# Kernel tuning notes

Measured on AMD Instinct MI355X. Metric: run time of the kernel, lower is better.

## Reference

```python
import jax, jax.numpy as jnp
import numpy as np

B, N, F_IN, HID, OUT = 4096, 116, 116, 256, 2


def setup_inputs() -> dict:
    key = jax.random.key(0)
    ks = jax.random.split(key, 10)
    x = jax.random.normal(ks[0], (B, N, F_IN), dtype=jnp.float32)
    support = jax.random.uniform(ks[1], (B, N, N), dtype=jnp.float32) / N  # row-normalized-ish adjacency
    s = 0.05
    W1 = jax.random.normal(ks[2], (F_IN, HID), dtype=jnp.float32) * s
    b1 = jnp.zeros((HID,), dtype=jnp.float32)
    W2 = jax.random.normal(ks[3], (HID, OUT * 2), dtype=jnp.float32) * s
    b2 = jnp.zeros((OUT * 2,), dtype=jnp.float32)
    Wr1 = jax.random.normal(ks[4], (N * OUT * 2, 64), dtype=jnp.float32) * s
    br1 = jnp.zeros((64,), dtype=jnp.float32)
    Wr2 = jax.random.normal(ks[5], (64, OUT), dtype=jnp.float32) * s
    br2 = jnp.zeros((OUT,), dtype=jnp.float32)
    return {"x": x, "support": support, "W1": W1, "b1": b1, "W2": W2,
            "b2": b2, "Wr1": Wr1, "br1": br1, "Wr2": Wr2, "br2": br2}


def graph_conv(x, support, W, b):
    # GraphConv: activation(support @ (x @ W) + b)
    xw = jnp.einsum('bnf,fh->bnh', x, W)
    h = jnp.einsum('bnm,bmh->bnh', support, xw) + b
    return jax.nn.relu(h)


def reference(x, support, W1, b1, W2, b2, Wr1, br1, Wr2, br2):
    h = graph_conv(x, support, W1, b1)          # [B, N, HID]
    h = graph_conv(h, support, W2, b2)          # [B, N, 2*OUT]
    flat = h.reshape(h.shape[0], -1)            # [B, N*2*OUT]
    r = jax.nn.relu(flat @ Wr1 + br1)           # [B, 64]
    logits = r @ Wr2 + br2                      # [B, OUT]
    return jax.nn.log_softmax(logits, axis=-1)
```

## Files before the change

kernel.cpp:

```cpp
#include <hip/hip_runtime.h>
#include <math.h>


#define BDIM 512

constexpr int Bsz = 4096;
constexpr int Nn  = 116;
constexpr int Fin = 116;
constexpr int HID = 256;
constexpr int SK  = 136;
constexpr int NF4 = 3364;
constexpr int W1T_ELEMS = 256 * SK;
constexpr int W2T_OFF   = W1T_ELEMS;

typedef __bf16 bf16;
typedef __bf16 bf16x4 __attribute__((ext_vector_type(4)));
typedef __bf16 bf16x8 __attribute__((ext_vector_type(8)));
typedef float  floatx4 __attribute__((ext_vector_type(4)));


__global__ __launch_bounds__(1024) void prep_weights(
    const float* __restrict__ W1, const float* __restrict__ W2,
    bf16* __restrict__ WT)
{
  int j = blockIdx.x * 1024 + threadIdx.x;
  if (j < W1T_ELEMS) {
    int h = j / SK, kk = j - h * SK;
    WT[j] = (bf16)((kk < Fin) ? W1[kk * HID + h] : 0.f);
  } else if (j < W1T_ELEMS + 4 * 264) {
    int t = j - W1T_ELEMS;
    int n = t / 264, k = t - n * 264;
    WT[j] = (bf16)((k < HID) ? W2[k * 4 + n] : 0.f);
  }
}

template <bool PADS>
__device__ __attribute__((always_inline)) inline void stage_mat(
    const float* __restrict__ g, bf16* dst, int tid)
{
  for (int i = tid; i < NF4; i += BDIM) {
    int m  = i / 29;
    int kq = (i - m * 29) * 4;
    float4 u = ((const float4*)g)[i];
    bf16x4 q; q[0]=(bf16)u.x; q[1]=(bf16)u.y; q[2]=(bf16)u.z; q[3]=(bf16)u.w;
    *(bf16x4*)&dst[m * SK + kq] = q;
  }
  if (PADS) {
    bf16x4 z; z[0]=z[1]=z[2]=z[3]=(bf16)0.f;
    for (int i = tid; i < 128 * 5; i += BDIM) {
      int m = i / 5, cc = 116 + (i - m * 5) * 4;
      *(bf16x4*)&dst[m * SK + cc] = z;
    }
    for (int i = tid; i < 12 * 29; i += BDIM) {
      int r = 116 + i / 29, cc = (i - (i / 29) * 29) * 4;
      *(bf16x4*)&dst[r * SK + cc] = z;
    }
  }
}

__device__ __attribute__((always_inline)) inline void gemm128(
    const bf16* A, const bf16* Bt, floatx4 (&acc)[2][4],
    int wm, int wn, int quad, int l16)
{
#pragma unroll
  for (int ks = 0; ks < 4; ++ks) {
    const int k0 = ks * 32 + quad * 8;
    bf16x8 af[2], bfr[4];
#pragma unroll
    for (int mt = 0; mt < 2; ++mt)
      af[mt] = *(const bf16x8*)&A[(wm + mt * 16 + l16) * SK + k0];
#pragma unroll
    for (int nt = 0; nt < 4; ++nt)
      bfr[nt] = *(const bf16x8*)&Bt[(wn + nt * 16 + l16) * SK + k0];
#pragma unroll
    for (int mt = 0; mt < 2; ++mt)
#pragma unroll
      for (int nt = 0; nt < 4; ++nt)
        acc[mt][nt] = __builtin_amdgcn_mfma_f32_16x16x32_bf16(af[mt], bfr[nt], acc[mt][nt], 0, 0, 0);
  }
}

__device__ __attribute__((always_inline)) inline void zero_acc(floatx4 (&acc)[2][4])
{
#pragma unroll
  for (int mt = 0; mt < 2; ++mt)
#pragma unroll
    for (int nt = 0; nt < 4; ++nt) { acc[mt][nt][0]=acc[mt][nt][1]=acc[mt][nt][2]=acc[mt][nt][3]=0.f; }
}

__global__ __launch_bounds__(BDIM, 4) void gcn_fused(
    const float* __restrict__ X, const float* __restrict__ SUPP,
    const bf16* __restrict__ WT,
    const float* __restrict__ B1v, const float* __restrict__ B2v,
    const float* __restrict__ Wr1, const float* __restrict__ br1,
    const float* __restrict__ Wr2, const float* __restrict__ br2,
    float* __restrict__ OUTP)
{
  __shared__ __align__(16) bf16 ssup[128 * SK];
  __shared__ __align__(16) bf16 swb [128 * SK];
  __shared__ __align__(16) bf16 sw2t[4 * 264];
  __shared__ __align__(16) bf16 stt [4 * SK];
  __shared__ float sh2[464];
  __shared__ float spart[8 * 64];

  const int b    = blockIdx.x;
  const int tid  = threadIdx.x;
  const int wid  = tid >> 6;
  const int lane = tid & 63;
  const int quad = lane >> 4;
  const int l16  = lane & 15;

  const int wm = (wid & 3) * 32;
  const int wn = (wid >> 2) * 64;

  stage_mat<true>(X + (size_t)b * (Nn * Fin), ssup, tid);
  for (int i = tid; i < 2176; i += BDIM)
    ((float4*)swb)[i] = ((const float4*)WT)[i];
  if (tid < 132) ((float4*)sw2t)[tid] = ((const float4*)(WT + W2T_OFF))[tid];
  __syncthreads();

  float4 w1pf[5];
#pragma unroll
  for (int j = 0; j < 5; ++j) {
    int i = tid + j * BDIM;
    if (i < 2176) w1pf[j] = ((const float4*)(WT + 128 * SK))[i];
  }

  floatx4 acc[2][4];
  bf16x4  xwb0[2][4], xwb1[2][4];

  zero_acc(acc);
  gemm128(ssup, swb, acc, wm, wn, quad, l16);
#pragma unroll
  for (int mt = 0; mt < 2; ++mt)
#pragma unroll
    for (int nt = 0; nt < 4; ++nt) {
      floatx4 a = acc[mt][nt];
      bf16x4 p; p[0]=(bf16)a[0]; p[1]=(bf16)a[1]; p[2]=(bf16)a[2]; p[3]=(bf16)a[3];
      xwb0[mt][nt] = p;
    }
  __syncthreads();
#pragma unroll
  for (int j = 0; j < 5; ++j) {
    int i = tid + j * BDIM;
    if (i < 2176) ((float4*)swb)[i] = w1pf[j];
  }
  __syncthreads();

  zero_acc(acc);
  gemm128(ssup, swb, acc, wm, wn, quad, l16);
#pragma unroll
  for (int mt = 0; mt < 2; ++mt)
#pragma unroll
    for (int nt = 0; nt < 4; ++nt) {
      floatx4 a = acc[mt][nt];
      bf16x4 p; p[0]=(bf16)a[0]; p[1]=(bf16)a[1]; p[2]=(bf16)a[2]; p[3]=(bf16)a[3];
      xwb1[mt][nt] = p;
    }
  __syncthreads();

  stage_mat<false>(SUPP + (size_t)b * (Nn * Nn), ssup, tid);
#pragma unroll
  for (int mt = 0; mt < 2; ++mt)
#pragma unroll
    for (int nt = 0; nt < 4; ++nt) {
      int mb = wm + mt * 16 + quad * 4;
      int n  = wn + nt * 16 + l16;
      *(bf16x4*)&swb[n * SK + mb] = xwb0[mt][nt];
    }
  __syncthreads();

  floatx4 acc3; acc3[0]=acc3[1]=acc3[2]=acc3[3]=0.f;

#pragma unroll
  for (int c = 0; c < 2; ++c) {
    zero_acc(acc);
    gemm128(ssup, swb, acc, wm, wn, quad, l16);
    __syncthreads();

#pragma unroll
    for (int mt = 0; mt < 2; ++mt)
#pragma unroll
      for (int nt = 0; nt < 4; ++nt) {
        int mb   = wm + mt * 16 + quad * 4;
        int coll = wn + nt * 16 + l16;
        float bb = B1v[c * 128 + coll];
        floatx4 a = acc[mt][nt];
#pragma unroll
        for (int r = 0; r < 4; ++r)
          swb[(mb + r) * SK + coll] = (bf16)fmaxf(a[r] + bb, 0.f);
      }
    __syncthreads();

#pragma unroll
    for (int ks = 0; ks < 4; ++ks) {
      const int k0 = ks * 32 + quad * 8;
      bf16x8 bfr = *(const bf16x8*)&sw2t[(l16 & 3) * 264 + c * 128 + k0];
      bf16x8 af  = *(const bf16x8*)&swb[(wid * 16 + l16) * SK + k0];
      acc3 = __builtin_amdgcn_mfma_f32_16x16x32_bf16(af, bfr, acc3, 0, 0, 0);
    }
    if (c == 0) {
      __syncthreads();
#pragma unroll
      for (int mt = 0; mt < 2; ++mt)
#pragma unroll
        for (int nt = 0; nt < 4; ++nt) {
          int mb = wm + mt * 16 + quad * 4;
          int n  = wn + nt * 16 + l16;
          *(bf16x4*)&swb[n * SK + mb] = xwb1[mt][nt];
        }
      __syncthreads();
    }
  }

  {
    int mb = wid * 16 + quad * 4;
    bf16x4 p;
    if (mb < Nn) { p[0]=(bf16)acc3[0]; p[1]=(bf16)acc3[1]; p[2]=(bf16)acc3[2]; p[3]=(bf16)acc3[3]; }
    else         { p[0]=p[1]=p[2]=p[3]=(bf16)0.f; }
    if (l16 < 4) *(bf16x4*)&stt[l16 * SK + mb] = p;
  }
  __syncthreads();

  floatx4 acc4; acc4[0]=acc4[1]=acc4[2]=acc4[3]=0.f;
#pragma unroll
  for (int ks = 0; ks < 4; ++ks) {
    const int k0 = ks * 32 + quad * 8;
    bf16x8 af  = *(const bf16x8*)&ssup[(wid * 16 + l16) * SK + k0];
    bf16x8 bfr = *(const bf16x8*)&stt[(l16 & 3) * SK + k0];
    acc4 = __builtin_amdgcn_mfma_f32_16x16x32_bf16(af, bfr, acc4, 0, 0, 0);
  }
  if (l16 < 4) {
    float bb = B2v[l16];
#pragma unroll
    for (int r = 0; r < 4; ++r) {
      int m = wid * 16 + quad * 4 + r;
      if (m < Nn) sh2[m * 4 + l16] = fmaxf(acc4[r] + bb, 0.f);
    }
  }
  __syncthreads();

  {
    int j   = tid & 63;
    int ksl = tid >> 6;
    int kb  = ksl * 58;
    float p = 0.f;
#pragma unroll 4
    for (int kk = 0; kk < 58; ++kk)
      p = fmaf(sh2[kb + kk], Wr1[(kb + kk) * 64 + j], p);
    spart[ksl * 64 + j] = p;
  }
  __syncthreads();
  if (tid < 64) {
    int j = tid;
    float r = 0.f;
#pragma unroll
    for (int s = 0; s < 8; ++s) r += spart[s * 64 + j];
    r = fmaxf(r + br1[j], 0.f);
    float p0 = r * Wr2[j * 2 + 0];
    float p1 = r * Wr2[j * 2 + 1];
#pragma unroll
    for (int off = 32; off > 0; off >>= 1) {
      p0 += __shfl_xor(p0, off, 64);
      p1 += __shfl_xor(p1, off, 64);
    }
    float l0 = p0 + br2[0], l1 = p1 + br2[1];
    float mx  = fmaxf(l0, l1);
    float lse = mx + logf(expf(l0 - mx) + expf(l1 - mx));
    if (j < 2) OUTP[(size_t)b * 2 + j] = (j ? l1 : l0) - lse;
  }
}

extern "C" void kernel_launch(void* const* d_in, const int* in_sizes, int n_in,
                              void* d_out, int out_size, void* d_ws, size_t ws_size,
                              hipStream_t stream) {
  const float* X    = (const float*)d_in[0];
  const float* SUPP = (const float*)d_in[1];
  const float* W1   = (const float*)d_in[2];
  const float* B1v  = (const float*)d_in[3];
  const float* W2   = (const float*)d_in[4];
  const float* B2v  = (const float*)d_in[5];
  const float* Wr1  = (const float*)d_in[6];
  const float* br1  = (const float*)d_in[7];
  const float* Wr2  = (const float*)d_in[8];
  const float* br2  = (const float*)d_in[9];
  bf16* WT = (bf16*)d_ws;

  prep_weights<<<36, 1024, 0, stream>>>(W1, W2, WT);
  gcn_fused<<<Bsz, BDIM, 0, stream>>>(X, SUPP, WT, B1v, B2v,
                                      Wr1, br1, Wr2, br2, (float*)d_out);
}
```

Measured before the change: 591.7 us.

## Keep X fragments in registers and stage weights via direct global-to-LDS loads

X rows are now loaded straight from global memory into per-wave register fragments for the X·W1 GEMMs, so X is no longer staged in LDS. This lets the support matrix be staged into LDS up front, overlapping with the weight loads. W1 halves are copied into LDS with global_load_lds (buffer-to-LDS DMA) instead of going through registers. The aim is to cut LDS round trips and register pressure from the prefetch array, at the cost of uncoalesced, strided per-lane X reads and explicit vmcnt waits.

```diff
diff --git a/kernel.cpp b/kernel.cpp
--- a/kernel.cpp
+++ b/kernel.cpp
@@ -34,28 +34,10 @@
   }
 }
 
-template <bool PADS>
-__device__ __attribute__((always_inline)) inline void stage_mat(
-    const float* __restrict__ g, bf16* dst, int tid)
-{
-  for (int i = tid; i < NF4; i += BDIM) {
-    int m  = i / 29;
-    int kq = (i - m * 29) * 4;
-    float4 u = ((const float4*)g)[i];
-    bf16x4 q; q[0]=(bf16)u.x; q[1]=(bf16)u.y; q[2]=(bf16)u.z; q[3]=(bf16)u.w;
-    *(bf16x4*)&dst[m * SK + kq] = q;
-  }
-  if (PADS) {
-    bf16x4 z; z[0]=z[1]=z[2]=z[3]=(bf16)0.f;
-    for (int i = tid; i < 128 * 5; i += BDIM) {
-      int m = i / 5, cc = 116 + (i - m * 5) * 4;
-      *(bf16x4*)&dst[m * SK + cc] = z;
-    }
-    for (int i = tid; i < 12 * 29; i += BDIM) {
-      int r = 116 + i / 29, cc = (i - (i / 29) * 29) * 4;
-      *(bf16x4*)&dst[r * SK + cc] = z;
-    }
-  }
+__device__ __forceinline__ void gl2lds16(const void* g, void* l) {
+  __builtin_amdgcn_global_load_lds(
+      (const __attribute__((address_space(1))) void*)g,
+      (__attribute__((address_space(3))) void*)l, 16, 0, 0);
 }
 
 __device__ __attribute__((always_inline)) inline void gemm128(
@@ -77,6 +59,25 @@
 #pragma unroll
       for (int nt = 0; nt < 4; ++nt)
         acc[mt][nt] = __builtin_amdgcn_mfma_f32_16x16x32_bf16(af[mt], bfr[nt], acc[mt][nt], 0, 0, 0);
+  }
+}
+
+__device__ __attribute__((always_inline)) inline void gemm128_ra(
+    const bf16x8 (&xf)[2][4], const bf16* Bt, floatx4 (&acc)[2][4],
+    int wn, int quad, int l16)
+{
+#pragma unroll
+  for (int ks = 0; ks < 4; ++ks) {
+    const int k0 = ks * 32 + quad * 8;
+    bf16x8 bfr[4];
+#pragma unroll
+    for (int nt = 0; nt < 4; ++nt)
+      bfr[nt] = *(const bf16x8*)&Bt[(wn + nt * 16 + l16) * SK + k0];
+#pragma unroll
+    for (int mt = 0; mt < 2; ++mt)
+#pragma unroll
+      for (int nt = 0; nt < 4; ++nt)
+        acc[mt][nt] = __builtin_amdgcn_mfma_f32_16x16x32_bf16(xf[mt][ks], bfr[nt], acc[mt][nt], 0, 0, 0);
   }
 }
 
@@ -113,24 +114,71 @@
   const int wm = (wid & 3) * 32;
   const int wn = (wid >> 2) * 64;
 
-  stage_mat<true>(X + (size_t)b * (Nn * Fin), ssup, tid);
-  for (int i = tid; i < 2176; i += BDIM)
-    ((float4*)swb)[i] = ((const float4*)WT)[i];
-  if (tid < 132) ((float4*)sw2t)[tid] = ((const float4*)(WT + W2T_OFF))[tid];
-  __syncthreads();
-
-  float4 w1pf[5];
-#pragma unroll
-  for (int j = 0; j < 5; ++j) {
-    int i = tid + j * BDIM;
-    if (i < 2176) w1pf[j] = ((const float4*)(WT + 128 * SK))[i];
-  }
+  {
+    const char* wg = (const char*)WT;
+    char* wl = (char*)swb;
+    for (int off = wid * 1024; off < 34816; off += 8 * 1024)
+      gl2lds16(wg + off + lane * 16, wl + off);
+    if (wid == 7) {
+      const char* w2g = (const char*)(WT + W2T_OFF);
+      char* w2l = (char*)sw2t;
+      gl2lds16(w2g + lane * 16, w2l);
+      gl2lds16(w2g + 1024 + lane * 16, w2l + 1024);
+      if (lane < 4) gl2lds16(w2g + 2048 + lane * 16, w2l + 2048);
+    }
+  }
+
+  const float* xrow = X + (size_t)b * (Nn * Fin);
+  bf16x8 xf[2][4];
+#pragma unroll
+  for (int mt = 0; mt < 2; ++mt) {
+    const int row = wm + mt * 16 + l16;
+    const bool rv = row < Nn;
+    const float* pr = xrow + (rv ? row : 0) * Fin;
+#pragma unroll
+    for (int ks = 0; ks < 4; ++ks) {
+      const int k0 = ks * 32 + quad * 8;
+      float4 u0 = make_float4(0.f, 0.f, 0.f, 0.f);
+      float4 u1 = make_float4(0.f, 0.f, 0.f, 0.f);
+      if (ks < 3 || quad < 3) u0 = *(const float4*)(pr + k0);
+      if (ks < 3 || quad < 2) u1 = *(const float4*)(pr + k0 + 4);
+      bf16x8 f;
+      f[0]=(bf16)u0.x; f[1]=(bf16)u0.y; f[2]=(bf16)u0.z; f[3]=(bf16)u0.w;
+      f[4]=(bf16)u1.x; f[5]=(bf16)u1.y; f[6]=(bf16)u1.z; f[7]=(bf16)u1.w;
+      bf16x8 z; 
+#pragma unroll
+      for (int j = 0; j < 8; ++j) z[j] = (bf16)0.f;
+      xf[mt][ks] = rv ? f : z;
+    }
+  }
+
+  {
+    const float4* sg = (const float4*)(SUPP + (size_t)b * (Nn * Nn));
+    for (int i = tid; i < NF4; i += BDIM) {
+      int m  = i / 29;
+      int kq = (i - m * 29) * 4;
+      float4 u = sg[i];
+      bf16x4 q; q[0]=(bf16)u.x; q[1]=(bf16)u.y; q[2]=(bf16)u.z; q[3]=(bf16)u.w;
+      *(bf16x4*)&ssup[m * SK + kq] = q;
+    }
+    bf16x4 z; z[0]=z[1]=z[2]=z[3]=(bf16)0.f;
+    for (int i = tid; i < 128 * 5; i += BDIM) {
+      int m = i / 5, cc = 116 + (i - m * 5) * 4;
+      *(bf16x4*)&ssup[m * SK + cc] = z;
+    }
+    for (int i = tid; i < 12 * 29; i += BDIM) {
+      int r = 116 + i / 29, cc = (i - (i / 29) * 29) * 4;
+      *(bf16x4*)&ssup[r * SK + cc] = z;
+    }
+  }
+  asm volatile("s_waitcnt vmcnt(0)" ::: "memory");
+  __syncthreads();
 
   floatx4 acc[2][4];
   bf16x4  xwb0[2][4], xwb1[2][4];
 
   zero_acc(acc);
-  gemm128(ssup, swb, acc, wm, wn, quad, l16);
+  gemm128_ra(xf, swb, acc, wn, quad, l16);
 #pragma unroll
   for (int mt = 0; mt < 2; ++mt)
 #pragma unroll
@@ -140,15 +188,18 @@
       xwb0[mt][nt] = p;
     }
   __syncthreads();
-#pragma unroll
-  for (int j = 0; j < 5; ++j) {
-    int i = tid + j * BDIM;
-    if (i < 2176) ((float4*)swb)[i] = w1pf[j];
-  }
+
+  {
+    const char* wg = (const char*)(WT + 128 * SK);
+    char* wl = (char*)swb;
+    for (int off = wid * 1024; off < 34816; off += 8 * 1024)
+      gl2lds16(wg + off + lane * 16, wl + off);
+  }
+  asm volatile("s_waitcnt vmcnt(0)" ::: "memory");
   __syncthreads();
 
   zero_acc(acc);
-  gemm128(ssup, swb, acc, wm, wn, quad, l16);
+  gemm128_ra(xf, swb, acc, wn, quad, l16);
 #pragma unroll
   for (int mt = 0; mt < 2; ++mt)
 #pragma unroll
@@ -159,7 +210,6 @@
     }
   __syncthreads();
 
-  stage_mat<false>(SUPP + (size_t)b * (Nn * Nn), ssup, tid);
 #pragma unroll
   for (int mt = 0; mt < 2; ++mt)
 #pragma unroll
```

After: 551.8 us. 6.7% less time.
